# Kernel optimization log

Measured on AMD Instinct MI355X. Metric: run time of the kernel, lower is better.

Reference implementation:

```python
import jax, jax.numpy as jnp
import numpy as np

N = 50000
E_RAND = 800000
IN_CH = 128
HID = 64
HEADS = 4
OUT_CH = 3
NEG_SLOPE = 0.2
BN_EPS = 1e-5


def setup_inputs() -> dict:
    key = jax.random.key(0)
    ks = jax.random.split(key, 24)
    x = jax.random.normal(ks[0], (N, IN_CH), dtype=jnp.float32)
    er = jax.random.randint(ks[1], (2, E_RAND), 0, N)
    sl = jnp.tile(jnp.arange(N, dtype=er.dtype)[None, :], (2, 1))
    edge_index = jnp.concatenate([er, sl], axis=1)  # [2, 850000]
    s = 0.1
    d1 = HID * HEADS            # 256
    d2 = (HID // 2) * HEADS     # 128
    inp = dict(x=x, edge_index=edge_index)
    # layer 1: in 128 -> heads*64
    inp["W1"] = s * jax.random.normal(ks[2], (IN_CH, HEADS * HID), dtype=jnp.float32)
    inp["a1s"] = s * jax.random.normal(ks[3], (HEADS, HID), dtype=jnp.float32)
    inp["a1d"] = s * jax.random.normal(ks[4], (HEADS, HID), dtype=jnp.float32)
    inp["b1"] = jnp.zeros((d1,), jnp.float32)
    inp["g1"] = jnp.ones((d1,), jnp.float32)
    inp["be1"] = jnp.zeros((d1,), jnp.float32)
    inp["m1"] = 0.01 * jax.random.normal(ks[5], (d1,), dtype=jnp.float32)
    inp["v1"] = jnp.ones((d1,), jnp.float32) + 0.01 * jax.random.uniform(ks[6], (d1,))
    # layer 2: in 256 -> heads*32
    inp["W2"] = s * jax.random.normal(ks[7], (d1, HEADS * (HID // 2)), dtype=jnp.float32)
    inp["a2s"] = s * jax.random.normal(ks[8], (HEADS, HID // 2), dtype=jnp.float32)
    inp["a2d"] = s * jax.random.normal(ks[9], (HEADS, HID // 2), dtype=jnp.float32)
    inp["b2"] = jnp.zeros((d2,), jnp.float32)
    inp["g2"] = jnp.ones((d2,), jnp.float32)
    inp["be2"] = jnp.zeros((d2,), jnp.float32)
    inp["m2"] = 0.01 * jax.random.normal(ks[10], (d2,), dtype=jnp.float32)
    inp["v2"] = jnp.ones((d2,), jnp.float32) + 0.01 * jax.random.uniform(ks[11], (d2,))
    # layer 3: in 128 -> 1 head, out_ch, concat=False
    inp["W3"] = s * jax.random.normal(ks[12], (d2, OUT_CH), dtype=jnp.float32)
    inp["a3s"] = s * jax.random.normal(ks[13], (1, OUT_CH), dtype=jnp.float32)
    inp["a3d"] = s * jax.random.normal(ks[14], (1, OUT_CH), dtype=jnp.float32)
    inp["b3"] = jnp.zeros((OUT_CH,), jnp.float32)
    return inp


def gat_conv(x, src, dst, W, a_src, a_dst, b, heads, fdim, concat):
    n = x.shape[0]
    h = (x @ W).reshape(n, heads, fdim)           # [N,H,F]
    als = jnp.einsum('nhf,hf->nh', h, a_src)      # [N,H]
    ald = jnp.einsum('nhf,hf->nh', h, a_dst)
    e = jax.nn.leaky_relu(als[src] + ald[dst], NEG_SLOPE)  # [E,H]
    m = jax.lax.stop_gradient(jax.ops.segment_max(e, dst, num_segments=n))
    ex = jnp.exp(e - m[dst])
    ssum = jax.ops.segment_sum(ex, dst, num_segments=n)
    alpha = ex / (ssum[dst] + 1e-16)              # segment softmax over in-edges
    msg = h[src] * alpha[:, :, None]              # [E,H,F]
    out = jax.ops.segment_sum(msg, dst, num_segments=n)  # [N,H,F]
    out = out.reshape(n, heads * fdim) if concat else out.mean(axis=1)
    return out + b


def batch_norm(x, gamma, beta, mean, var):
    return (x - mean) * jax.lax.rsqrt(var + BN_EPS) * gamma + beta


def reference(x, edge_index, W1, a1s, a1d, b1, g1, be1, m1, v1,
              W2, a2s, a2d, b2, g2, be2, m2, v2,
              W3, a3s, a3d, b3):
    src, dst = edge_index[0], edge_index[1]
    h = gat_conv(x, src, dst, W1, a1s, a1d, b1, HEADS, HID, True)
    h = jax.nn.elu(batch_norm(h, g1, be1, m1, v1))
    h = gat_conv(h, src, dst, W2, a2s, a2d, b2, HEADS, HID // 2, True)
    h = jax.nn.elu(batch_norm(h, g2, be2, m2, v2))
    h = gat_conv(h, src, dst, W3, a3s, a3d, b3, 1, OUT_CH, False)
    return jax.nn.log_softmax(h, axis=1)
```

## Files before the change

kernel.cpp:

```cpp
#include <hip/hip_runtime.h>


#define WSZ 64

typedef short short8 __attribute__((ext_vector_type(8)));
typedef float float4v __attribute__((ext_vector_type(4)));

__device__ inline unsigned short f2bf(float f) {
  unsigned u = __float_as_uint(f);
  u += 0x7FFFu + ((u >> 16) & 1u);
  return (unsigned short)(u >> 16);
}


__global__ __launch_bounds__(256) void hist_kernel(const int* __restrict__ dst, int E,
                                                   int* __restrict__ deg) {
  int e = blockIdx.x * 256 + threadIdx.x;
  if (e < E) atomicAdd(&deg[dst[e]], 1);
}

__global__ __launch_bounds__(256) void block_sums_kernel(const int* __restrict__ deg, int n,
                                                         int* __restrict__ bsum) {
  __shared__ int sh[256];
  int t = threadIdx.x;
  int base = blockIdx.x * 1024 + t * 4;
  int v = 0;
#pragma unroll
  for (int j = 0; j < 4; ++j) {
    int idx = base + j;
    if (idx < n) v += deg[idx];
  }
  sh[t] = v;
  __syncthreads();
  for (int off = 128; off >= 1; off >>= 1) {
    if (t < off) sh[t] += sh[t + off];
    __syncthreads();
  }
  if (t == 0) bsum[blockIdx.x] = sh[0];
}

__global__ void scan_blocks_kernel(int* bsum, int nb) {
  int lane = threadIdx.x & 63;
  int orig = (lane < nb) ? bsum[lane] : 0;
  int v = orig;
#pragma unroll
  for (int off = 1; off < 64; off <<= 1) {
    int o = __shfl_up(v, off, 64);
    if (lane >= off) v += o;
  }
  if (lane < nb) bsum[lane] = v - orig;
}

__global__ __launch_bounds__(256) void scan_write_kernel(const int* __restrict__ deg, int n,
                                                         const int* __restrict__ bbase,
                                                         int* __restrict__ row_start,
                                                         int* __restrict__ cursor) {
  __shared__ int sh[256];
  int t = threadIdx.x;
  int base = blockIdx.x * 1024 + t * 4;
  int v[4];
  int s = 0;
#pragma unroll
  for (int j = 0; j < 4; ++j) {
    int idx = base + j;
    v[j] = (idx < n) ? deg[idx] : 0;
    s += v[j];
  }
  sh[t] = s;
  __syncthreads();
  for (int off = 1; off < 256; off <<= 1) {
    int x = (t >= off) ? sh[t - off] : 0;
    __syncthreads();
    sh[t] += x;
    __syncthreads();
  }
  int excl = sh[t] - s + bbase[blockIdx.x];
#pragma unroll
  for (int j = 0; j < 4; ++j) {
    int idx = base + j;
    if (idx < n) {
      row_start[idx] = excl;
      cursor[idx] = excl;
    }
    excl += v[j];
  }
  if (blockIdx.x == gridDim.x - 1 && t == 255) row_start[n] = excl;
}

__global__ __launch_bounds__(256) void scatter_kernel(const int* __restrict__ src,
                                                      const int* __restrict__ dst, int E,
                                                      int* __restrict__ cursor,
                                                      int* __restrict__ csr_src) {
  int e = blockIdx.x * 256 + threadIdx.x;
  if (e < E) {
    int d = dst[e];
    int p = atomicAdd(&cursor[d], 1);
    csr_src[p] = src[e];
  }
}

__global__ __launch_bounds__(256) void conv_weights_kernel(const float* __restrict__ W1,
                                                           const float* __restrict__ W2,
                                                           unsigned short* __restrict__ W1t,
                                                           unsigned short* __restrict__ W2t) {
  int b = blockIdx.x;
  if (b < 128) {
    int idx = b * 256 + threadIdx.x;
    int n = idx >> 7, k = idx & 127;
    W1t[idx] = f2bf(W1[k * 256 + n]);
  } else {
    int idx = (b - 128) * 256 + threadIdx.x;
    int n = idx >> 8, p = idx & 255;
    int kl = (p & ~63) | ((p & 3) << 4) | ((p >> 2) & 15);
    W2t[idx] = f2bf(W2[kl * 128 + n]);
  }
}


template <int K, int NTOT, bool AF32>
__global__ __launch_bounds__(256) void gemm_mfma2(
    const void* __restrict__ Ap,
    const unsigned short* __restrict__ Bt,
    const float* __restrict__ a_s, const float* __restrict__ a_d,
    unsigned short* __restrict__ hout,
    float* __restrict__ als, float* __restrict__ ald,
    int M) {
  constexpr int COLS = NTOT / 2;
  constexpr int CFW = COLS / 16;
  constexpr int HLOG = NTOT / 4;
  constexpr int CFH = HLOG / 16;
  constexpr int VPT = NTOT / 64;
  constexpr int KS = K / 32;
  __shared__ __align__(16) unsigned short Bs[COLS][K + 8];

  const int t = threadIdx.x;
  const int w = t >> 6;
  const int lane = t & 63;
  const int c16 = lane & 15;
  const int q = lane >> 4;
  const int gcol = blockIdx.y;
  const int bm = blockIdx.x * 128;

  {
    constexpr int TPR = K / 64;
    int nloc = t / TPR;
    int part = (t % TPR) * 64;
    const unsigned short* srcp = Bt + (size_t)(gcol * COLS + nloc) * K + part;
#pragma unroll
    for (int j = 0; j < 8; ++j) {
      uint4 v = *(const uint4*)(srcp + j * 8);
      *(uint4*)&Bs[nloc][part + j * 8] = v;
    }
  }

  int arow[2];
  arow[0] = min(bm + w * 32 + c16, M - 1);
  arow[1] = min(bm + w * 32 + 16 + c16, M - 1);
  short8 afr[2][KS];
  if constexpr (AF32) {
    float4 fv[2][KS][2];
#pragma unroll
    for (int rf = 0; rf < 2; ++rf) {
      const float* rp = (const float*)Ap + (size_t)arow[rf] * K;
#pragma unroll
      for (int ks = 0; ks < KS; ++ks) {
        fv[rf][ks][0] = *(const float4*)(rp + ks * 32 + q * 8);
        fv[rf][ks][1] = *(const float4*)(rp + ks * 32 + q * 8 + 4);
      }
    }
#pragma unroll
    for (int rf = 0; rf < 2; ++rf)
#pragma unroll
      for (int ks = 0; ks < KS; ++ks) {
        ushort4 u0, u1;
        u0.x = f2bf(fv[rf][ks][0].x); u0.y = f2bf(fv[rf][ks][0].y);
        u0.z = f2bf(fv[rf][ks][0].z); u0.w = f2bf(fv[rf][ks][0].w);
        u1.x = f2bf(fv[rf][ks][1].x); u1.y = f2bf(fv[rf][ks][1].y);
        u1.z = f2bf(fv[rf][ks][1].z); u1.w = f2bf(fv[rf][ks][1].w);
        union { ushort4 u[2]; short8 s; } cvt;
        cvt.u[0] = u0; cvt.u[1] = u1;
        afr[rf][ks] = cvt.s;
      }
  } else {
    const unsigned short* Ab = (const unsigned short*)Ap;
#pragma unroll
    for (int rf = 0; rf < 2; ++rf)
#pragma unroll
      for (int ks = 0; ks < KS; ++ks)
        afr[rf][ks] = *(const short8*)(Ab + (size_t)arow[rf] * K + ks * 32 + q * 8);
  }
  __syncthreads();

  float4v acc[2][CFW];
#pragma unroll
  for (int rf = 0; rf < 2; ++rf)
#pragma unroll
    for (int cf = 0; cf < CFW; ++cf) acc[rf][cf] = float4v{0.f, 0.f, 0.f, 0.f};

#pragma unroll
  for (int ks = 0; ks < KS; ++ks) {
#pragma unroll
    for (int cf = 0; cf < CFW; ++cf) {
      short8 bfrag = *(const short8*)&Bs[cf * 16 + c16][ks * 32 + q * 8];
#pragma unroll
      for (int rf = 0; rf < 2; ++rf)
        acc[rf][cf] =
            __builtin_amdgcn_mfma_f32_16x16x32_bf16(afr[rf][ks], bfrag, acc[rf][cf], 0, 0, 0);
    }
  }

  float sasv[CFW], sadv[CFW];
#pragma unroll
  for (int cf = 0; cf < CFW; ++cf) {
    int L = gcol * COLS + cf * 16 + c16;
    sasv[cf] = a_s[L];
    sadv[cf] = a_d[L];
  }
#pragma unroll
  for (int rf = 0; rf < 2; ++rf) {
#pragma unroll
    for (int r = 0; r < 4; ++r) {
      int n = bm + w * 32 + rf * 16 + q * 4 + r;
      float ps[2] = {0.f, 0.f}, pd[2] = {0.f, 0.f};
      unsigned short us[CFW];
#pragma unroll
      for (int cf = 0; cf < CFW; ++cf) {
        float v = acc[rf][cf][r];
        us[cf] = f2bf(v);
        ps[cf / CFH] += v * sasv[cf];
        pd[cf / CFH] += v * sadv[cf];
      }
#pragma unroll
      for (int off = 1; off <= 8; off <<= 1) {
#pragma unroll
        for (int hl = 0; hl < 2; ++hl) {
          ps[hl] += __shfl_xor(ps[hl], off, 16);
          pd[hl] += __shfl_xor(pd[hl], off, 16);
        }
      }
      if (n < M) {
#pragma unroll
        for (int hl = 0; hl < 2; ++hl) {
          int head = gcol * 2 + hl;
          unsigned short* dst = hout + (size_t)n * NTOT + head * HLOG + c16 * VPT;
          if constexpr (VPT == 4) {
            ushort4 u;
            u.x = us[hl * 4 + 0]; u.y = us[hl * 4 + 1];
            u.z = us[hl * 4 + 2]; u.w = us[hl * 4 + 3];
            *(ushort4*)dst = u;
          } else {
            ushort2 u;
            u.x = us[hl * 2 + 0]; u.y = us[hl * 2 + 1];
            *(ushort2*)dst = u;
          }
          if (c16 == 0) {
            als[(size_t)n * 4 + head] = ps[hl];
            ald[(size_t)n * 4 + head] = pd[hl];
          }
        }
      }
    }
  }
}


template <int D, bool FUSEL3>
__global__ __launch_bounds__(256) void gat_aggregate(
    const unsigned short* __restrict__ h_bf, const float* __restrict__ als,
    const float* __restrict__ ald, const int* __restrict__ row_start,
    const int* __restrict__ csr_src, const float* __restrict__ bias,
    const float* __restrict__ gamma, const float* __restrict__ beta,
    const float* __restrict__ bmean, const float* __restrict__ bvar,
    unsigned short* __restrict__ obf,
    const float* __restrict__ W3, const float* __restrict__ a3s,
    const float* __restrict__ a3d, float4* __restrict__ h3p,
    float* __restrict__ ald3,
    int n_nodes) {
  constexpr int VPT = D / WSZ;
  constexpr int H = 4;
  __shared__ float w3s[384];
  __shared__ float sa3[6];
  if constexpr (FUSEL3) {
    for (int i = threadIdx.x; i < 384; i += 256) w3s[i] = W3[i];
    if (threadIdx.x < 3) {
      sa3[threadIdx.x] = a3s[threadIdx.x];
      sa3[3 + threadIdx.x] = a3d[threadIdx.x];
    }
    __syncthreads();
  }
  int wid = threadIdx.x >> 6, lane = threadIdx.x & 63;
  int n = blockIdx.x * 4 + wid;
  if (n >= n_nodes) return;
  int c = lane * VPT;
  int hd = lane >> 4;
  float aldv = ald[(size_t)n * H + hd];
  int row = row_start[n], end = row_start[n + 1];
  float acc[VPT] = {};
  float ssum = 0.f;
  int i = row;

#define EDGE_BLOCK(B)                                                          \
  for (; i + (B) - 1 < end; i += (B)) {                                        \
    int s[B];                                                                  \
    float e[B];                                                                \
    _Pragma("unroll") for (int j = 0; j < (B); ++j) s[j] = csr_src[i + j];     \
    _Pragma("unroll") for (int j = 0; j < (B); ++j) e[j] =                     \
        als[(size_t)s[j] * H + hd] + aldv;                                     \
    if constexpr (VPT == 4) {                                                  \
      uint2 u[B];                                                              \
      _Pragma("unroll") for (int j = 0; j < (B); ++j) u[j] =                   \
          *(const uint2*)(h_bf + (size_t)s[j] * D + c);                        \
      _Pragma("unroll") for (int j = 0; j < (B); ++j) {                        \
        float ee = e[j];                                                       \
        ee = (ee > 0.f) ? ee : 0.2f * ee;                                      \
        float ex = __expf(ee);                                                 \
        ssum += ex;                                                            \
        acc[0] += ex * __uint_as_float(u[j].x << 16);                          \
        acc[1] += ex * __uint_as_float(u[j].x & 0xFFFF0000u);                  \
        acc[2] += ex * __uint_as_float(u[j].y << 16);                          \
        acc[3] += ex * __uint_as_float(u[j].y & 0xFFFF0000u);                  \
      }                                                                        \
    } else {                                                                   \
      unsigned u[B];                                                           \
      _Pragma("unroll") for (int j = 0; j < (B); ++j) u[j] =                   \
          *(const unsigned*)(h_bf + (size_t)s[j] * D + c);                     \
      _Pragma("unroll") for (int j = 0; j < (B); ++j) {                        \
        float ee = e[j];                                                       \
        ee = (ee > 0.f) ? ee : 0.2f * ee;                                      \
        float ex = __expf(ee);                                                 \
        ssum += ex;                                                            \
        acc[0] += ex * __uint_as_float(u[j] << 16);                            \
        acc[1] += ex * __uint_as_float(u[j] & 0xFFFF0000u);                    \
      }                                                                        \
    }                                                                          \
  }

  EDGE_BLOCK(8)
  EDGE_BLOCK(4)
  EDGE_BLOCK(1)
#undef EDGE_BLOCK

  float inv = 1.f / (ssum + 1e-16f);
#pragma unroll
  for (int j = 0; j < VPT; ++j) {
    int cl = hd * (VPT * 16) + j * 16 + (lane & 15);
    float o = acc[j] * inv + bias[cl];
    o = (o - bmean[cl]) * rsqrtf(bvar[cl] + 1e-5f) * gamma[cl] + beta[cl];
    o = (o > 0.f) ? o : (__expf(o) - 1.f);
    acc[j] = o;
  }
  if constexpr (!FUSEL3) {
    ushort4 u;
    u.x = f2bf(acc[0]); u.y = f2bf(acc[1]); u.z = f2bf(acc[2]); u.w = f2bf(acc[3]);
    *(ushort4*)(obf + (size_t)n * D + c) = u;
  } else {
    int k0l = hd * 32 + (lane & 15);
    int k1l = k0l + 16;
    float p0 = acc[0] * w3s[k0l * 3 + 0] + acc[1] * w3s[k1l * 3 + 0];
    float p1 = acc[0] * w3s[k0l * 3 + 1] + acc[1] * w3s[k1l * 3 + 1];
    float p2 = acc[0] * w3s[k0l * 3 + 2] + acc[1] * w3s[k1l * 3 + 2];
#pragma unroll
    for (int off = 32; off >= 1; off >>= 1) {
      p0 += __shfl_xor(p0, off, 64);
      p1 += __shfl_xor(p1, off, 64);
      p2 += __shfl_xor(p2, off, 64);
    }
    if (lane == 0) {
      float als3 = p0 * sa3[0] + p1 * sa3[1] + p2 * sa3[2];
      float ad3 = p0 * sa3[3] + p1 * sa3[4] + p2 * sa3[5];
      h3p[n] = make_float4(p0, p1, p2, als3);
      ald3[n] = ad3;
    }
  }
}


__global__ __launch_bounds__(256) void l3_agg_kernel(const float4* __restrict__ h3p,
                                                     const float* __restrict__ ald3,
                                                     const int* __restrict__ row_start,
                                                     const int* __restrict__ csr_src,
                                                     const float* __restrict__ b3,
                                                     float* __restrict__ out, int n_nodes) {
  int wid = threadIdx.x >> 6, lane = threadIdx.x & 63;
  int n = blockIdx.x * 4 + wid;
  if (n >= n_nodes) return;
  float aldv = ald3[n];
  int row = row_start[n], end = row_start[n + 1];
  float a0 = 0.f, a1 = 0.f, a2 = 0.f, ss = 0.f;
  for (int i = row + lane; i < end; i += 64) {
    int s = csr_src[i];
    float4 hv = h3p[s];
    float e = hv.w + aldv;
    e = (e > 0.f) ? e : 0.2f * e;
    float ex = __expf(e);
    ss += ex;
    a0 += ex * hv.x;
    a1 += ex * hv.y;
    a2 += ex * hv.z;
  }
#pragma unroll
  for (int off = 32; off >= 1; off >>= 1) {
    a0 += __shfl_xor(a0, off, 64);
    a1 += __shfl_xor(a1, off, 64);
    a2 += __shfl_xor(a2, off, 64);
    ss += __shfl_xor(ss, off, 64);
  }
  if (lane == 0) {
    float inv = 1.f / (ss + 1e-16f);
    float o0 = a0 * inv + b3[0];
    float o1 = a1 * inv + b3[1];
    float o2 = a2 * inv + b3[2];
    float m = fmaxf(o0, fmaxf(o1, o2));
    float lse = m + logf(expf(o0 - m) + expf(o1 - m) + expf(o2 - m));
    out[n * 3 + 0] = o0 - lse;
    out[n * 3 + 1] = o1 - lse;
    out[n * 3 + 2] = o2 - lse;
  }
}


extern "C" void kernel_launch(void* const* d_in, const int* in_sizes, int n_in,
                              void* d_out, int out_size, void* d_ws, size_t ws_size,
                              hipStream_t stream) {
  const float* x   = (const float*)d_in[0];
  const int*   ei  = (const int*)d_in[1];
  const float* W1  = (const float*)d_in[2];
  const float* a1s = (const float*)d_in[3];
  const float* a1d = (const float*)d_in[4];
  const float* b1  = (const float*)d_in[5];
  const float* g1v = (const float*)d_in[6];
  const float* be1 = (const float*)d_in[7];
  const float* m1  = (const float*)d_in[8];
  const float* v1  = (const float*)d_in[9];
  const float* W2  = (const float*)d_in[10];
  const float* a2s = (const float*)d_in[11];
  const float* a2d = (const float*)d_in[12];
  const float* b2  = (const float*)d_in[13];
  const float* g2v = (const float*)d_in[14];
  const float* be2 = (const float*)d_in[15];
  const float* m2  = (const float*)d_in[16];
  const float* v2  = (const float*)d_in[17];
  const float* W3  = (const float*)d_in[18];
  const float* a3s = (const float*)d_in[19];
  const float* a3d = (const float*)d_in[20];
  const float* b3  = (const float*)d_in[21];
  float* out = (float*)d_out;

  const int N = in_sizes[0] / 128;
  const int E = in_sizes[1] / 2;
  const int* srcv = ei;
  const int* dstv = ei + E;

  float* wsf  = (float*)d_ws;
  float* als1 = wsf;
  float* ald1 = als1 + (size_t)N * 4;
  float* als2 = ald1 + (size_t)N * 4;
  float* ald2 = als2 + (size_t)N * 4;
  float* h3p  = ald2 + (size_t)N * 4;
  float* ald3 = h3p + (size_t)N * 4;
  unsigned short* h_bf1 = (unsigned short*)(ald3 + N);
  unsigned short* o1_bf = h_bf1 + (size_t)N * 256;
  unsigned short* h_bf2 = o1_bf + (size_t)N * 256;
  unsigned short* W1t   = h_bf2 + (size_t)N * 128;
  unsigned short* W2t   = W1t + 256 * 128;
  int* deg       = (int*)(W2t + 128 * 256);
  int* row_start = deg + N;
  int* cursor    = row_start + (N + 1);
  int* csr_src   = cursor + (N + 1);
  int* bsum      = csr_src + E;

  const int eb = (E + 255) / 256;
  const int nb = (N + 1023) / 1024;
  const int nodes4 = (N + 3) / 4;
  const dim3 gemm_grid((N + 127) / 128, 2);

  conv_weights_kernel<<<256, 256, 0, stream>>>(W1, W2, W1t, W2t);

  hipMemsetAsync(deg, 0, (size_t)N * sizeof(int), stream);
  hist_kernel<<<eb, 256, 0, stream>>>(dstv, E, deg);
  block_sums_kernel<<<nb, 256, 0, stream>>>(deg, N, bsum);
  scan_blocks_kernel<<<1, 64, 0, stream>>>(bsum, nb);
  scan_write_kernel<<<nb, 256, 0, stream>>>(deg, N, bsum, row_start, cursor);
  scatter_kernel<<<eb, 256, 0, stream>>>(srcv, dstv, E, cursor, csr_src);

  gemm_mfma2<128, 256, true><<<gemm_grid, 256, 0, stream>>>(x, W1t, a1s, a1d, h_bf1, als1,
                                                            ald1, N);
  gat_aggregate<256, false><<<nodes4, 256, 0, stream>>>(
      h_bf1, als1, ald1, row_start, csr_src, b1, g1v, be1, m1, v1, o1_bf, nullptr, nullptr,
      nullptr, nullptr, nullptr, N);
  gemm_mfma2<256, 128, false><<<gemm_grid, 256, 0, stream>>>(o1_bf, W2t, a2s, a2d, h_bf2,
                                                             als2, ald2, N);
  gat_aggregate<128, true><<<nodes4, 256, 0, stream>>>(
      h_bf2, als2, ald2, row_start, csr_src, b2, g2v, be2, m2, v2, nullptr, W3, a3s, a3d,
      (float4*)h3p, ald3, N);
  l3_agg_kernel<<<nodes4, 256, 0, stream>>>((const float4*)h3p, ald3, row_start, csr_src,
                                            b3, out, N);
}
```

Measured before the change: 383.6 us.

## Merge CSR build kernels with weight conversion and GEMM1, narrow layer-3 aggregation

Folds the weight bf16 conversion into the degree-histogram kernel and replaces the three-kernel prefix scan with a single 1024-thread block scan. The CSR scatter and the first GEMM now run in one launch, with block indices partitioning the two jobs so they can overlap. The layer-3 aggregation uses 16 lanes per node instead of 64, which matches the low average degree. The aim is to cut launch count and idle tail time, at the cost of a serial single-block scan where each thread walks about 49 entries.

```diff
diff --git a/kernel.cpp b/kernel.cpp
--- a/kernel.cpp
+++ b/kernel.cpp
@@ -13,118 +13,64 @@
 }
 
 
-__global__ __launch_bounds__(256) void hist_kernel(const int* __restrict__ dst, int E,
-                                                   int* __restrict__ deg) {
-  int e = blockIdx.x * 256 + threadIdx.x;
-  if (e < E) atomicAdd(&deg[dst[e]], 1);
-}
-
-__global__ __launch_bounds__(256) void block_sums_kernel(const int* __restrict__ deg, int n,
-                                                         int* __restrict__ bsum) {
-  __shared__ int sh[256];
-  int t = threadIdx.x;
-  int base = blockIdx.x * 1024 + t * 4;
-  int v = 0;
-#pragma unroll
-  for (int j = 0; j < 4; ++j) {
-    int idx = base + j;
-    if (idx < n) v += deg[idx];
-  }
-  sh[t] = v;
-  __syncthreads();
-  for (int off = 128; off >= 1; off >>= 1) {
-    if (t < off) sh[t] += sh[t + off];
-    __syncthreads();
-  }
-  if (t == 0) bsum[blockIdx.x] = sh[0];
-}
-
-__global__ void scan_blocks_kernel(int* bsum, int nb) {
-  int lane = threadIdx.x & 63;
-  int orig = (lane < nb) ? bsum[lane] : 0;
-  int v = orig;
-#pragma unroll
-  for (int off = 1; off < 64; off <<= 1) {
-    int o = __shfl_up(v, off, 64);
-    if (lane >= off) v += o;
-  }
-  if (lane < nb) bsum[lane] = v - orig;
-}
-
-__global__ __launch_bounds__(256) void scan_write_kernel(const int* __restrict__ deg, int n,
-                                                         const int* __restrict__ bbase,
-                                                         int* __restrict__ row_start,
-                                                         int* __restrict__ cursor) {
-  __shared__ int sh[256];
-  int t = threadIdx.x;
-  int base = blockIdx.x * 1024 + t * 4;
-  int v[4];
-  int s = 0;
-#pragma unroll
-  for (int j = 0; j < 4; ++j) {
-    int idx = base + j;
-    v[j] = (idx < n) ? deg[idx] : 0;
-    s += v[j];
-  }
-  sh[t] = s;
-  __syncthreads();
-  for (int off = 1; off < 256; off <<= 1) {
-    int x = (t >= off) ? sh[t - off] : 0;
-    __syncthreads();
-    sh[t] += x;
-    __syncthreads();
-  }
-  int excl = sh[t] - s + bbase[blockIdx.x];
-#pragma unroll
-  for (int j = 0; j < 4; ++j) {
-    int idx = base + j;
-    if (idx < n) {
-      row_start[idx] = excl;
-      cursor[idx] = excl;
-    }
-    excl += v[j];
-  }
-  if (blockIdx.x == gridDim.x - 1 && t == 255) row_start[n] = excl;
-}
-
-__global__ __launch_bounds__(256) void scatter_kernel(const int* __restrict__ src,
-                                                      const int* __restrict__ dst, int E,
-                                                      int* __restrict__ cursor,
-                                                      int* __restrict__ csr_src) {
-  int e = blockIdx.x * 256 + threadIdx.x;
-  if (e < E) {
-    int d = dst[e];
-    int p = atomicAdd(&cursor[d], 1);
-    csr_src[p] = src[e];
-  }
-}
-
-__global__ __launch_bounds__(256) void conv_weights_kernel(const float* __restrict__ W1,
-                                                           const float* __restrict__ W2,
-                                                           unsigned short* __restrict__ W1t,
-                                                           unsigned short* __restrict__ W2t) {
+__global__ __launch_bounds__(256) void conv_hist_kernel(
+    const float* __restrict__ W1, const float* __restrict__ W2,
+    unsigned short* __restrict__ W1t, unsigned short* __restrict__ W2t,
+    const int* __restrict__ dst, int E, int* __restrict__ deg) {
   int b = blockIdx.x;
   if (b < 128) {
     int idx = b * 256 + threadIdx.x;
     int n = idx >> 7, k = idx & 127;
     W1t[idx] = f2bf(W1[k * 256 + n]);
-  } else {
-    int idx = (b - 128) * 256 + threadIdx.x;
+  } else if (b < 256) {
+    int idx = (b - 256 + 128) * 256 + threadIdx.x;
     int n = idx >> 8, p = idx & 255;
     int kl = (p & ~63) | ((p & 3) << 4) | ((p >> 2) & 15);
     W2t[idx] = f2bf(W2[kl * 128 + n]);
-  }
+  } else {
+    int e = (b - 256) * 256 + threadIdx.x;
+    if (e < E) atomicAdd(&deg[dst[e]], 1);
+  }
+}
+
+
+__global__ __launch_bounds__(1024) void scan_all_kernel(const int* __restrict__ deg, int n,
+                                                        int* __restrict__ row_start,
+                                                        int* __restrict__ cursor) {
+  __shared__ int sh[1024];
+  int t = threadIdx.x;
+  const int per = (n + 1023) / 1024;
+  int base = t * per;
+  int cnt = n - base;
+  if (cnt < 0) cnt = 0;
+  if (cnt > per) cnt = per;
+  int s = 0;
+  for (int j = 0; j < cnt; ++j) s += deg[base + j];
+  sh[t] = s;
+  __syncthreads();
+  for (int off = 1; off < 1024; off <<= 1) {
+    int x = (t >= off) ? sh[t - off] : 0;
+    __syncthreads();
+    sh[t] += x;
+    __syncthreads();
+  }
+  int run = sh[t] - s;
+  for (int j = 0; j < cnt; ++j) {
+    int idx = base + j;
+    row_start[idx] = run;
+    cursor[idx] = run;
+    run += deg[idx];
+  }
+  if (t == 1023) row_start[n] = sh[1023];
 }
 
 
 template <int K, int NTOT, bool AF32>
-__global__ __launch_bounds__(256) void gemm_mfma2(
-    const void* __restrict__ Ap,
-    const unsigned short* __restrict__ Bt,
+__device__ __forceinline__ void gemm_body(
+    const void* __restrict__ Ap, const unsigned short* __restrict__ Bt,
     const float* __restrict__ a_s, const float* __restrict__ a_d,
-    unsigned short* __restrict__ hout,
-    float* __restrict__ als, float* __restrict__ ald,
-    int M) {
+    unsigned short* __restrict__ hout, float* __restrict__ als, float* __restrict__ ald,
+    int M, int bm, int gcol) {
   constexpr int COLS = NTOT / 2;
   constexpr int CFW = COLS / 16;
   constexpr int HLOG = NTOT / 4;
@@ -138,8 +84,6 @@
   const int lane = t & 63;
   const int c16 = lane & 15;
   const int q = lane >> 4;
-  const int gcol = blockIdx.y;
-  const int bm = blockIdx.x * 128;
 
   {
     constexpr int TPR = K / 64;
@@ -242,16 +186,16 @@
 #pragma unroll
         for (int hl = 0; hl < 2; ++hl) {
           int head = gcol * 2 + hl;
-          unsigned short* dst = hout + (size_t)n * NTOT + head * HLOG + c16 * VPT;
+          unsigned short* dstp = hout + (size_t)n * NTOT + head * HLOG + c16 * VPT;
           if constexpr (VPT == 4) {
             ushort4 u;
             u.x = us[hl * 4 + 0]; u.y = us[hl * 4 + 1];
             u.z = us[hl * 4 + 2]; u.w = us[hl * 4 + 3];
-            *(ushort4*)dst = u;
+            *(ushort4*)dstp = u;
           } else {
             ushort2 u;
             u.x = us[hl * 2 + 0]; u.y = us[hl * 2 + 1];
-            *(ushort2*)dst = u;
+            *(ushort2*)dstp = u;
           }
           if (c16 == 0) {
             als[(size_t)n * 4 + head] = ps[hl];
@@ -261,6 +205,39 @@
       }
     }
   }
+}
+
+
+__global__ __launch_bounds__(256) void scatter_gemm1_kernel(
+    const int* __restrict__ src, const int* __restrict__ dst, int E,
+    int* __restrict__ cursor, int* __restrict__ csr_src,
+    const float* __restrict__ x, const unsigned short* __restrict__ W1t,
+    const float* __restrict__ a1s, const float* __restrict__ a1d,
+    unsigned short* __restrict__ h_bf1, float* __restrict__ als1,
+    float* __restrict__ ald1, int M, int sblocks, int mblocks) {
+  if ((int)blockIdx.x < sblocks) {
+    int e = blockIdx.x * 256 + threadIdx.x;
+    if (e < E) {
+      int d = dst[e];
+      int p = atomicAdd(&cursor[d], 1);
+      csr_src[p] = src[e];
+    }
+  } else {
+    int g = blockIdx.x - sblocks;
+    int bm = (g % mblocks) * 128;
+    int gcol = g / mblocks;
+    gemm_body<128, 256, true>(x, W1t, a1s, a1d, h_bf1, als1, ald1, M, bm, gcol);
+  }
+}
+
+
+__global__ __launch_bounds__(256) void gemm2_kernel(
+    const unsigned short* __restrict__ o1_bf, const unsigned short* __restrict__ W2t,
+    const float* __restrict__ a2s, const float* __restrict__ a2d,
+    unsigned short* __restrict__ h_bf2, float* __restrict__ als2,
+    float* __restrict__ ald2, int M) {
+  gemm_body<256, 128, false>(o1_bf, W2t, a2s, a2d, h_bf2, als2, ald2, M,
+                             blockIdx.x * 128, blockIdx.y);
 }
 
 
@@ -382,30 +359,34 @@
                                                      const float* __restrict__ b3,
                                                      float* __restrict__ out, int n_nodes) {
   int wid = threadIdx.x >> 6, lane = threadIdx.x & 63;
-  int n = blockIdx.x * 4 + wid;
-  if (n >= n_nodes) return;
-  float aldv = ald3[n];
-  int row = row_start[n], end = row_start[n + 1];
+  int sub = lane >> 4, l16 = lane & 15;
+  int n = blockIdx.x * 16 + wid * 4 + sub;
+  bool ok = (n < n_nodes);
   float a0 = 0.f, a1 = 0.f, a2 = 0.f, ss = 0.f;
-  for (int i = row + lane; i < end; i += 64) {
-    int s = csr_src[i];
-    float4 hv = h3p[s];
-    float e = hv.w + aldv;
-    e = (e > 0.f) ? e : 0.2f * e;
-    float ex = __expf(e);
-    ss += ex;
-    a0 += ex * hv.x;
-    a1 += ex * hv.y;
-    a2 += ex * hv.z;
-  }
-#pragma unroll
-  for (int off = 32; off >= 1; off >>= 1) {
-    a0 += __shfl_xor(a0, off, 64);
-    a1 += __shfl_xor(a1, off, 64);
-    a2 += __shfl_xor(a2, off, 64);
-    ss += __shfl_xor(ss, off, 64);
-  }
-  if (lane == 0) {
+  float aldv = 0.f;
+  if (ok) {
+    aldv = ald3[n];
+    int row = row_start[n], end = row_start[n + 1];
+    for (int i = row + l16; i < end; i += 16) {
+      int s = csr_src[i];
+      float4 hv = h3p[s];
+      float e = hv.w + aldv;
+      e = (e > 0.f) ? e : 0.2f * e;
+      float ex = __expf(e);
+      ss += ex;
+      a0 += ex * hv.x;
+      a1 += ex * hv.y;
+      a2 += ex * hv.z;
+    }
+  }
+#pragma unroll
+  for (int off = 1; off <= 8; off <<= 1) {
+    a0 += __shfl_xor(a0, off, 16);
+    a1 += __shfl_xor(a1, off, 16);
+    a2 += __shfl_xor(a2, off, 16);
+    ss += __shfl_xor(ss, off, 16);
+  }
+  if (ok && l16 == 0) {
     float inv = 1.f / (ss + 1e-16f);
     float o0 = a0 * inv + b3[0];
     float o1 = a1 * inv + b3[1];
@@ -467,32 +448,24 @@
   int* row_start = deg + N;
   int* cursor    = row_start + (N + 1);
   int* csr_src   = cursor + (N + 1);
-  int* bsum      = csr_src + E;
 
   const int eb = (E + 255) / 256;
-  const int nb = (N + 1023) / 1024;
   const int nodes4 = (N + 3) / 4;
-  const dim3 gemm_grid((N + 127) / 128, 2);
-
-  conv_weights_kernel<<<256, 256, 0, stream>>>(W1, W2, W1t, W2t);
+  const int mblocks = (N + 127) / 128;
 
   hipMemsetAsync(deg, 0, (size_t)N * sizeof(int), stream);
-  hist_kernel<<<eb, 256, 0, stream>>>(dstv, E, deg);
-  block_sums_kernel<<<nb, 256, 0, stream>>>(deg, N, bsum);
-  scan_blocks_kernel<<<1, 64, 0, stream>>>(bsum, nb);
-  scan_write_kernel<<<nb, 256, 0, stream>>>(deg, N, bsum, row_start, cursor);
-  scatter_kernel<<<eb, 256, 0, stream>>>(srcv, dstv, E, cursor, csr_src);
-
-  gemm_mfma2<128, 256, true><<<gemm_grid, 256, 0, stream>>>(x, W1t, a1s, a1d, h_bf1, als1,
-                                                            ald1, N);
+  conv_hist_kernel<<<256 + eb, 256, 0, stream>>>(W1, W2, W1t, W2t, dstv, E, deg);
+  scan_all_kernel<<<1, 1024, 0, stream>>>(deg, N, row_start, cursor);
+  scatter_gemm1_kernel<<<eb + 2 * mblocks, 256, 0, stream>>>(
+      srcv, dstv, E, cursor, csr_src, x, W1t, a1s, a1d, h_bf1, als1, ald1, N, eb, mblocks);
   gat_aggregate<256, false><<<nodes4, 256, 0, stream>>>(
       h_bf1, als1, ald1, row_start, csr_src, b1, g1v, be1, m1, v1, o1_bf, nullptr, nullptr,
       nullptr, nullptr, nullptr, N);
-  gemm_mfma2<256, 128, false><<<gemm_grid, 256, 0, stream>>>(o1_bf, W2t, a2s, a2d, h_bf2,
-                                                             als2, ald2, N);
+  gemm2_kernel<<<dim3(mblocks, 2), 256, 0, stream>>>(o1_bf, W2t, a2s, a2d, h_bf2, als2,
+                                                     ald2, N);
   gat_aggregate<128, true><<<nodes4, 256, 0, stream>>>(
       h_bf2, als2, ald2, row_start, csr_src, b2, g2v, be2, m2, v2, nullptr, W3, a3s, a3d,
       (float4*)h3p, ald3, N);
-  l3_agg_kernel<<<nodes4, 256, 0, stream>>>((const float4*)h3p, ald3, row_start, csr_src,
-                                            b3, out, N);
-}
+  l3_agg_kernel<<<(N + 15) / 16, 256, 0, stream>>>((const float4*)h3p, ald3, row_start,
+                                                   csr_src, b3, out, N);
+}
```

Result: slower. 482.3 us (+25.7%).
